# Kernel optimization log

Measured on AMD Instinct MI355X. Metric: run time of the kernel, lower is better.

The kernel has to match this reference:

```python
import jax, jax.numpy as jnp
import numpy as np

N, D, M1, K = 16384, 128, 64, 8  # batch, nodes (dims[0]), dims[1], k


def setup_inputs() -> dict:
    key = jax.random.key(0)
    ks = jax.random.split(key, 8)
    x = jax.random.normal(ks[0], (N, D), dtype=jnp.float32)
    # Stacked per-node fc1 weights: d independent Linear(d, m1) layers.
    s = 0.1
    w1_pos = jax.random.normal(ks[1], (D, M1, D), dtype=jnp.float32) * s
    b1_pos = jax.random.normal(ks[2], (D, M1), dtype=jnp.float32) * s
    w1_neg = jax.random.normal(ks[3], (D, M1, D), dtype=jnp.float32) * s
    b1_neg = jax.random.normal(ks[4], (D, M1), dtype=jnp.float32) * s
    # LocallyConnected(K, M1, 1): weight [K, M1, 1], bias [K, 1]
    w2 = jax.random.normal(ks[5], (K, M1, 1), dtype=jnp.float32) * s
    b2 = jax.random.normal(ks[6], (K, 1), dtype=jnp.float32) * s
    # fc3: d independent Linear(K, 1, bias=False) -> stacked [D, K]
    w3 = jax.random.normal(ks[7], (D, K), dtype=jnp.float32) * s
    return {"x": x, "w1_pos": w1_pos, "b1_pos": b1_pos,
            "w1_neg": w1_neg, "b1_neg": b1_neg,
            "w2": w2, "b2": b2, "w3": w3}


def reference(x, w1_pos, b1_pos, w1_neg, b1_neg, w2, b2, w3):
    d = x.shape[1]
    # Zeroing x[:, j] for node j == zeroing column j of node-j fc1 weight.
    mask = 1.0 - jnp.eye(d, dtype=x.dtype)            # [d, d]
    W = (w1_pos - w1_neg) * mask[:, None, :]          # [d, m1, d]
    b = b1_pos - b1_neg                                # [d, m1]
    h = jnp.einsum('nd,jmd->njm', x, W) + b            # [n, d, m1]
    # expand over K then sigmoid (sigmoid is identical for each k copy)
    h = jax.nn.sigmoid(h)
    # LocallyConnected: per-k matmul [m1 -> 1], bias [K, 1]
    z = jnp.einsum('njm,kmo->njko', h, w2) + b2        # [n, d, K, 1]
    z = z[..., 0]                                       # [n, d, K]
    # fc3: per-node Linear(K, 1, bias=False)
    out = jnp.einsum('njk,jk->nj', z, w3)              # [n, d]
    return out
```

## Files before the change

kernel.cpp:

```cpp
#include <hip/hip_runtime.h>
#include <hip/hip_bf16.h>

#define N_  16384
#define D_  128
#define M1_ 64
#define K_  8
#define LOG2E 1.44269504088896f

typedef short short8 __attribute__((ext_vector_type(8)));
typedef float f32x4  __attribute__((ext_vector_type(4)));

__device__ __forceinline__ ushort f2bf(float f) {
    union { float f; unsigned u; } un; un.f = f;
    unsigned u = un.u;
    return (ushort)((u + 0x7fffu + ((u >> 16) & 1u)) >> 16);
}

__global__ void prep_all(const float* __restrict__ x,
                         const float* __restrict__ w1p, const float* __restrict__ b1p,
                         const float* __restrict__ w1n, const float* __restrict__ b1n,
                         const float* __restrict__ w2,  const float* __restrict__ b2,
                         const float* __restrict__ w3,
                         ushort* __restrict__ xbf, ushort* __restrict__ wbf,
                         float* __restrict__ bp, float* __restrict__ vv,
                         float* __restrict__ cv) {
    int bx = blockIdx.x;
    if (bx < 2048) {
        int i = bx * 256 + threadIdx.x;
        int n = i >> 5;
        int d = (i & 31) * 4;
        float4 f = ((const float4*)x)[i];
        ushort4 o;
        o.x = f2bf(f.x); o.y = f2bf(f.y); o.z = f2bf(f.z); o.w = f2bf(f.w);
        int lane = (n & 15) + 16 * ((d >> 3) & 3);
        int idx  = (n >> 4) * 2048 + (d >> 5) * 512 + lane * 8 + (d & 7);
        *(ushort4*)&xbf[idx] = o;
    } else if (bx < 3072) {
        int i = (bx - 2048) * 256 + threadIdx.x;
        int base = i * 4;
        int j   = base >> 13;
        int rem = base & 8191;
        int m   = rem >> 7;
        int d   = rem & 127;
        float4 p = ((const float4*)w1p)[i];
        float4 n = ((const float4*)w1n)[i];
        float4 w;
        w.x = (p.x - n.x) * LOG2E; w.y = (p.y - n.y) * LOG2E;
        w.z = (p.z - n.z) * LOG2E; w.w = (p.w - n.w) * LOG2E;
        if (j == d    ) w.x = 0.f;
        if (j == d + 1) w.y = 0.f;
        if (j == d + 2) w.z = 0.f;
        if (j == d + 3) w.w = 0.f;
        ushort4 o;
        o.x = f2bf(w.x); o.y = f2bf(w.y); o.z = f2bf(w.z); o.w = f2bf(w.w);
        int lane = (m & 15) + 16 * ((d >> 3) & 3);
        int idx  = j * 8192 + ((d >> 5) * 4 + (m >> 4)) * 512 + lane * 8 + (d & 7);
        *(ushort4*)&wbf[idx] = o;
    } else {
        int idx = (bx - 3072) * 256 + threadIdx.x;
        int j = idx >> 6, m = idx & 63;
        float v = 0.f;
        for (int k = 0; k < K_; k++) v += w3[j * K_ + k] * w2[k * M1_ + m];
        vv[idx] = v;
        bp[idx] = (b1p[idx] - b1n[idx]) * LOG2E;
        if (m == 0) {
            float c = 0.f;
            for (int k = 0; k < K_; k++) c += w3[j * K_ + k] * b2[k];
            cv[j] = c;
        }
    }
}

__global__ __launch_bounds__(256) void main_mfma(
    const ushort* __restrict__ xbf, const ushort* __restrict__ wbf,
    const float* __restrict__ bvec, const float* __restrict__ vvec,
    const float* __restrict__ cvec, float* __restrict__ out) {
    const int tid  = threadIdx.x;
    const int wave = tid >> 6, lane = tid & 63;
    const int quad = lane >> 4, col = lane & 15;
    const int j    = blockIdx.y;
    const int nblk = blockIdx.x;

    short8 wfrag[4][4];
    const ushort* wg = wbf + (size_t)j * 8192 + lane * 8;
    #pragma unroll
    for (int ks = 0; ks < 4; ks++)
        #pragma unroll
        for (int mt = 0; mt < 4; mt++)
            wfrag[mt][ks] = *(const short8*)&wg[(ks * 4 + mt) * 512];

    f32x4 bias4[4], vm4[4];
    #pragma unroll
    for (int mt = 0; mt < 4; mt++) {
        bias4[mt] = *(const f32x4*)&bvec[j * M1_ + mt * 16 + quad * 4];
        vm4[mt]   = *(const f32x4*)&vvec[j * M1_ + mt * 16 + quad * 4];
    }
    const float cj = cvec[j];

    const ushort* xg = xbf + ((size_t)(nblk * 32 + wave)) * 2048 + lane * 8;
    float* outp = out + (size_t)(nblk * 512 + wave * 16 + col) * D_ + j;

    short8 abuf[2][4];
    #pragma unroll
    for (int ks = 0; ks < 4; ks++)
        abuf[0][ks] = *(const short8*)&xg[ks * 512];

    float pr[8];

    #pragma unroll
    for (int st = 0; st < 8; st++) {
        const int cur = st & 1, nxt = cur ^ 1;
        if (st < 7) {
            const ushort* xn = xg + (size_t)(st + 1) * 8192;
            #pragma unroll
            for (int ks = 0; ks < 4; ks++)
                abuf[nxt][ks] = *(const short8*)&xn[ks * 512];
        }

        f32x4 acc[4];
        #pragma unroll
        for (int mt = 0; mt < 4; mt++) acc[mt] = bias4[mt];
        #pragma unroll
        for (int ks = 0; ks < 4; ks++)
            #pragma unroll
            for (int mt = 0; mt < 4; mt++)
                acc[mt] = __builtin_amdgcn_mfma_f32_16x16x32_bf16(
                              wfrag[mt][ks], abuf[cur][ks], acc[mt], 0, 0, 0);

        float partial = 0.f;
        #pragma unroll
        for (int mt = 0; mt < 4; mt++)
            #pragma unroll
            for (int r = 0; r < 4; r++) {
                float e = __builtin_amdgcn_exp2f(-acc[mt][r]);
                float s = __builtin_amdgcn_rcpf(1.0f + e);
                partial = fmaf(s, vm4[mt][r], partial);
            }
        pr[st] = partial;
    }

    #pragma unroll
    for (int st = 0; st < 8; st++)
        pr[st] += __shfl_xor(pr[st], 16);
    #pragma unroll
    for (int st = 0; st < 8; st++)
        pr[st] += __shfl_xor(pr[st], 32);
    if (quad == 0) {
        #pragma unroll
        for (int st = 0; st < 8; st++)
            outp[(size_t)st * 64 * D_] = pr[st] + cj;
    }
}

__global__ void fallback_kernel(const float* __restrict__ x,
                                const float* __restrict__ w1p, const float* __restrict__ b1p,
                                const float* __restrict__ w1n, const float* __restrict__ b1n,
                                const float* __restrict__ w2,  const float* __restrict__ b2,
                                const float* __restrict__ w3,  float* __restrict__ out) {
    int n = blockIdx.x, j = blockIdx.y, m = threadIdx.x;
    const float* xr = x + (size_t)n * D_;
    const float* wp = w1p + ((size_t)j * M1_ + m) * D_;
    const float* wn = w1n + ((size_t)j * M1_ + m) * D_;
    float acc = 0.f;
    for (int d = 0; d < D_; d++) {
        if (d == j) continue;
        acc += xr[d] * (wp[d] - wn[d]);
    }
    acc += b1p[j * M1_ + m] - b1n[j * M1_ + m];
    float h = 1.f / (1.f + __expf(-acc));
    float vmv = 0.f;
    for (int k = 0; k < K_; k++) vmv += w3[j * K_ + k] * w2[k * M1_ + m];
    float p = h * vmv;
    for (int off = 1; off < 64; off <<= 1) p += __shfl_xor(p, off);
    if (m == 0) {
        float c = 0.f;
        for (int k = 0; k < K_; k++) c += w3[j * K_ + k] * b2[k];
        out[(size_t)n * D_ + j] = p + c;
    }
}

extern "C" void kernel_launch(void* const* d_in, const int* in_sizes, int n_in,
                              void* d_out, int out_size, void* d_ws, size_t ws_size,
                              hipStream_t stream) {
    const float* x   = (const float*)d_in[0];
    const float* w1p = (const float*)d_in[1];
    const float* b1p = (const float*)d_in[2];
    const float* w1n = (const float*)d_in[3];
    const float* b1n = (const float*)d_in[4];
    const float* w2  = (const float*)d_in[5];
    const float* b2  = (const float*)d_in[6];
    const float* w3  = (const float*)d_in[7];
    float* out = (float*)d_out;

    const size_t off_x = 0;
    const size_t off_w = off_x + (size_t)N_ * D_ * 2;
    const size_t off_b = off_w + (size_t)D_ * M1_ * D_ * 2;
    const size_t off_v = off_b + (size_t)D_ * M1_ * 4;
    const size_t off_c = off_v + (size_t)D_ * M1_ * 4;
    const size_t need  = off_c + (size_t)D_ * 4;

    if (ws_size < need) {
        fallback_kernel<<<dim3(N_, D_), 64, 0, stream>>>(x, w1p, b1p, w1n, b1n, w2, b2, w3, out);
        return;
    }

    ushort* xbf = (ushort*)((char*)d_ws + off_x);
    ushort* wbf = (ushort*)((char*)d_ws + off_w);
    float*  bp  = (float*)((char*)d_ws + off_b);
    float*  vv  = (float*)((char*)d_ws + off_v);
    float*  cv  = (float*)((char*)d_ws + off_c);

    prep_all<<<3104, 256, 0, stream>>>(x, w1p, b1p, w1n, b1n, w2, b2, w3,
                                       xbf, wbf, bp, vv, cv);
    main_mfma<<<dim3(32, 128), 256, 0, stream>>>(xbf, wbf, bp, vv, cv, out);
}
```

Baseline: 124.1 us.

## Fuse bf16 prep into main MFMA kernel, converting x and weights on the fly

Removes the separate prep kernel and workspace. The main kernel now reads fp32 x and the w1 weights directly, converts them to bf16 in registers with the packed cvt instruction, and computes the bias, v and c vectors per block. It also shares a single reciprocal across four sigmoids through product tricks. This saves a launch and the workspace round trip. In exchange each of the 128 j-blocks re-reads fp32 x (twice the bytes of bf16), and each of the 32 n-blocks redundantly converts the same weights.

```diff
diff --git a/kernel.cpp b/kernel.cpp
--- a/kernel.cpp
+++ b/kernel.cpp
@@ -1,5 +1,4 @@
 #include <hip/hip_runtime.h>
-#include <hip/hip_bf16.h>
 
 #define N_  16384
 #define D_  128
@@ -10,71 +9,19 @@
 typedef short short8 __attribute__((ext_vector_type(8)));
 typedef float f32x4  __attribute__((ext_vector_type(4)));
 
-__device__ __forceinline__ ushort f2bf(float f) {
-    union { float f; unsigned u; } un; un.f = f;
-    unsigned u = un.u;
-    return (ushort)((u + 0x7fffu + ((u >> 16) & 1u)) >> 16);
+__device__ __forceinline__ unsigned cvt_pk_bf16(float lo, float hi) {
+    unsigned r;
+    asm("v_cvt_pk_bf16_f32 %0, %1, %2" : "=v"(r) : "v"(lo), "v"(hi));
+    return r;
 }
 
-__global__ void prep_all(const float* __restrict__ x,
-                         const float* __restrict__ w1p, const float* __restrict__ b1p,
-                         const float* __restrict__ w1n, const float* __restrict__ b1n,
-                         const float* __restrict__ w2,  const float* __restrict__ b2,
-                         const float* __restrict__ w3,
-                         ushort* __restrict__ xbf, ushort* __restrict__ wbf,
-                         float* __restrict__ bp, float* __restrict__ vv,
-                         float* __restrict__ cv) {
-    int bx = blockIdx.x;
-    if (bx < 2048) {
-        int i = bx * 256 + threadIdx.x;
-        int n = i >> 5;
-        int d = (i & 31) * 4;
-        float4 f = ((const float4*)x)[i];
-        ushort4 o;
-        o.x = f2bf(f.x); o.y = f2bf(f.y); o.z = f2bf(f.z); o.w = f2bf(f.w);
-        int lane = (n & 15) + 16 * ((d >> 3) & 3);
-        int idx  = (n >> 4) * 2048 + (d >> 5) * 512 + lane * 8 + (d & 7);
-        *(ushort4*)&xbf[idx] = o;
-    } else if (bx < 3072) {
-        int i = (bx - 2048) * 256 + threadIdx.x;
-        int base = i * 4;
-        int j   = base >> 13;
-        int rem = base & 8191;
-        int m   = rem >> 7;
-        int d   = rem & 127;
-        float4 p = ((const float4*)w1p)[i];
-        float4 n = ((const float4*)w1n)[i];
-        float4 w;
-        w.x = (p.x - n.x) * LOG2E; w.y = (p.y - n.y) * LOG2E;
-        w.z = (p.z - n.z) * LOG2E; w.w = (p.w - n.w) * LOG2E;
-        if (j == d    ) w.x = 0.f;
-        if (j == d + 1) w.y = 0.f;
-        if (j == d + 2) w.z = 0.f;
-        if (j == d + 3) w.w = 0.f;
-        ushort4 o;
-        o.x = f2bf(w.x); o.y = f2bf(w.y); o.z = f2bf(w.z); o.w = f2bf(w.w);
-        int lane = (m & 15) + 16 * ((d >> 3) & 3);
-        int idx  = j * 8192 + ((d >> 5) * 4 + (m >> 4)) * 512 + lane * 8 + (d & 7);
-        *(ushort4*)&wbf[idx] = o;
-    } else {
-        int idx = (bx - 3072) * 256 + threadIdx.x;
-        int j = idx >> 6, m = idx & 63;
-        float v = 0.f;
-        for (int k = 0; k < K_; k++) v += w3[j * K_ + k] * w2[k * M1_ + m];
-        vv[idx] = v;
-        bp[idx] = (b1p[idx] - b1n[idx]) * LOG2E;
-        if (m == 0) {
-            float c = 0.f;
-            for (int k = 0; k < K_; k++) c += w3[j * K_ + k] * b2[k];
-            cv[j] = c;
-        }
-    }
-}
-
-__global__ __launch_bounds__(256) void main_mfma(
-    const ushort* __restrict__ xbf, const ushort* __restrict__ wbf,
-    const float* __restrict__ bvec, const float* __restrict__ vvec,
-    const float* __restrict__ cvec, float* __restrict__ out) {
+__global__ __launch_bounds__(256) void fused_all(
+    const float* __restrict__ x,
+    const float* __restrict__ w1p, const float* __restrict__ b1p,
+    const float* __restrict__ w1n, const float* __restrict__ b1n,
+    const float* __restrict__ w2,  const float* __restrict__ b2,
+    const float* __restrict__ w3,  float* __restrict__ out)
+{
     const int tid  = threadIdx.x;
     const int wave = tid >> 6, lane = tid & 63;
     const int quad = lane >> 4, col = lane & 15;
@@ -82,39 +29,90 @@
     const int nblk = blockIdx.x;
 
     short8 wfrag[4][4];
-    const ushort* wg = wbf + (size_t)j * 8192 + lane * 8;
+    {
+        const float* wp = w1p + ((size_t)j * M1_ + col) * D_ + quad * 8;
+        const float* wn = w1n + ((size_t)j * M1_ + col) * D_ + quad * 8;
+        #pragma unroll
+        for (int mt = 0; mt < 4; mt++) {
+            #pragma unroll
+            for (int ks = 0; ks < 4; ks++) {
+                const size_t o = (size_t)mt * 16 * D_ + ks * 32;
+                float4 p0 = *(const float4*)(wp + o);
+                float4 p1 = *(const float4*)(wp + o + 4);
+                float4 n0 = *(const float4*)(wn + o);
+                float4 n1 = *(const float4*)(wn + o + 4);
+                float f[8];
+                f[0] = p0.x - n0.x; f[1] = p0.y - n0.y;
+                f[2] = p0.z - n0.z; f[3] = p0.w - n0.w;
+                f[4] = p1.x - n1.x; f[5] = p1.y - n1.y;
+                f[6] = p1.z - n1.z; f[7] = p1.w - n1.w;
+                const int dbase = ks * 32 + quad * 8;
+                #pragma unroll
+                for (int e = 0; e < 8; e++)
+                    f[e] = (dbase + e == j) ? 0.f : f[e] * LOG2E;
+                union { unsigned u[4]; short8 s; } r;
+                r.u[0] = cvt_pk_bf16(f[0], f[1]);
+                r.u[1] = cvt_pk_bf16(f[2], f[3]);
+                r.u[2] = cvt_pk_bf16(f[4], f[5]);
+                r.u[3] = cvt_pk_bf16(f[6], f[7]);
+                wfrag[mt][ks] = r.s;
+            }
+        }
+    }
+
+    float w3v[K_];
     #pragma unroll
-    for (int ks = 0; ks < 4; ks++)
-        #pragma unroll
-        for (int mt = 0; mt < 4; mt++)
-            wfrag[mt][ks] = *(const short8*)&wg[(ks * 4 + mt) * 512];
+    for (int k = 0; k < K_; k++) w3v[k] = w3[j * K_ + k];
 
     f32x4 bias4[4], vm4[4];
     #pragma unroll
     for (int mt = 0; mt < 4; mt++) {
-        bias4[mt] = *(const f32x4*)&bvec[j * M1_ + mt * 16 + quad * 4];
-        vm4[mt]   = *(const f32x4*)&vvec[j * M1_ + mt * 16 + quad * 4];
+        #pragma unroll
+        for (int r = 0; r < 4; r++) {
+            const int m = mt * 16 + quad * 4 + r;
+            float v = 0.f;
+            #pragma unroll
+            for (int k = 0; k < K_; k++) v = fmaf(w3v[k], w2[k * M1_ + m], v);
+            vm4[mt][r]   = v;
+            bias4[mt][r] = (b1p[j * M1_ + m] - b1n[j * M1_ + m]) * LOG2E;
+        }
     }
-    const float cj = cvec[j];
+    float cj = 0.f;
+    #pragma unroll
+    for (int k = 0; k < K_; k++) cj = fmaf(w3v[k], b2[k], cj);
 
-    const ushort* xg = xbf + ((size_t)(nblk * 32 + wave)) * 2048 + lane * 8;
+    const float* xg = x + ((size_t)((nblk * 32 + wave) * 16 + col)) * D_ + quad * 8;
     float* outp = out + (size_t)(nblk * 512 + wave * 16 + col) * D_ + j;
 
-    short8 abuf[2][4];
+    float4 raw[8];
     #pragma unroll
-    for (int ks = 0; ks < 4; ks++)
-        abuf[0][ks] = *(const short8*)&xg[ks * 512];
+    for (int ks = 0; ks < 4; ks++) {
+        raw[2 * ks]     = *(const float4*)(xg + ks * 32);
+        raw[2 * ks + 1] = *(const float4*)(xg + ks * 32 + 4);
+    }
 
     float pr[8];
 
     #pragma unroll
     for (int st = 0; st < 8; st++) {
-        const int cur = st & 1, nxt = cur ^ 1;
+        short8 abuf[4];
+        #pragma unroll
+        for (int ks = 0; ks < 4; ks++) {
+            union { unsigned u[4]; short8 s; } r;
+            r.u[0] = cvt_pk_bf16(raw[2 * ks].x,     raw[2 * ks].y);
+            r.u[1] = cvt_pk_bf16(raw[2 * ks].z,     raw[2 * ks].w);
+            r.u[2] = cvt_pk_bf16(raw[2 * ks + 1].x, raw[2 * ks + 1].y);
+            r.u[3] = cvt_pk_bf16(raw[2 * ks + 1].z, raw[2 * ks + 1].w);
+            abuf[ks] = r.s;
+        }
+
         if (st < 7) {
-            const ushort* xn = xg + (size_t)(st + 1) * 8192;
+            const float* xn = xg + (size_t)(st + 1) * (4 * 16 * D_);
             #pragma unroll
-            for (int ks = 0; ks < 4; ks++)
-                abuf[nxt][ks] = *(const short8*)&xn[ks * 512];
+            for (int ks = 0; ks < 4; ks++) {
+                raw[2 * ks]     = *(const float4*)(xn + ks * 32);
+                raw[2 * ks + 1] = *(const float4*)(xn + ks * 32 + 4);
+            }
         }
 
         f32x4 acc[4];
@@ -125,26 +123,30 @@
             #pragma unroll
             for (int mt = 0; mt < 4; mt++)
                 acc[mt] = __builtin_amdgcn_mfma_f32_16x16x32_bf16(
-                              wfrag[mt][ks], abuf[cur][ks], acc[mt], 0, 0, 0);
+                              wfrag[mt][ks], abuf[ks], acc[mt], 0, 0, 0);
 
         float partial = 0.f;
         #pragma unroll
-        for (int mt = 0; mt < 4; mt++)
-            #pragma unroll
-            for (int r = 0; r < 4; r++) {
-                float e = __builtin_amdgcn_exp2f(-acc[mt][r]);
-                float s = __builtin_amdgcn_rcpf(1.0f + e);
-                partial = fmaf(s, vm4[mt][r], partial);
-            }
+        for (int mt = 0; mt < 4; mt++) {
+            float e0 = __builtin_amdgcn_exp2f(-acc[mt][0]);
+            float e1 = __builtin_amdgcn_exp2f(-acc[mt][1]);
+            float e2 = __builtin_amdgcn_exp2f(-acc[mt][2]);
+            float e3 = __builtin_amdgcn_exp2f(-acc[mt][3]);
+            float u0 = 1.f + e0, u1 = 1.f + e1, u2 = 1.f + e2, u3 = 1.f + e3;
+            float p01 = u0 * u1, p23 = u2 * u3;
+            float rc  = __builtin_amdgcn_rcpf(p01 * p23);
+            partial = fmaf(vm4[mt][0], rc * (p23 * u1), partial);
+            partial = fmaf(vm4[mt][1], rc * (p23 * u0), partial);
+            partial = fmaf(vm4[mt][2], rc * (p01 * u3), partial);
+            partial = fmaf(vm4[mt][3], rc * (p01 * u2), partial);
+        }
         pr[st] = partial;
     }
 
     #pragma unroll
-    for (int st = 0; st < 8; st++)
-        pr[st] += __shfl_xor(pr[st], 16);
+    for (int st = 0; st < 8; st++) pr[st] += __shfl_xor(pr[st], 16);
     #pragma unroll
-    for (int st = 0; st < 8; st++)
-        pr[st] += __shfl_xor(pr[st], 32);
+    for (int st = 0; st < 8; st++) pr[st] += __shfl_xor(pr[st], 32);
     if (quad == 0) {
         #pragma unroll
         for (int st = 0; st < 8; st++)
@@ -152,65 +154,14 @@
     }
 }
 
-__global__ void fallback_kernel(const float* __restrict__ x,
-                                const float* __restrict__ w1p, const float* __restrict__ b1p,
-                                const float* __restrict__ w1n, const float* __restrict__ b1n,
-                                const float* __restrict__ w2,  const float* __restrict__ b2,
-                                const float* __restrict__ w3,  float* __restrict__ out) {
-    int n = blockIdx.x, j = blockIdx.y, m = threadIdx.x;
-    const float* xr = x + (size_t)n * D_;
-    const float* wp = w1p + ((size_t)j * M1_ + m) * D_;
-    const float* wn = w1n + ((size_t)j * M1_ + m) * D_;
-    float acc = 0.f;
-    for (int d = 0; d < D_; d++) {
-        if (d == j) continue;
-        acc += xr[d] * (wp[d] - wn[d]);
-    }
-    acc += b1p[j * M1_ + m] - b1n[j * M1_ + m];
-    float h = 1.f / (1.f + __expf(-acc));
-    float vmv = 0.f;
-    for (int k = 0; k < K_; k++) vmv += w3[j * K_ + k] * w2[k * M1_ + m];
-    float p = h * vmv;
-    for (int off = 1; off < 64; off <<= 1) p += __shfl_xor(p, off);
-    if (m == 0) {
-        float c = 0.f;
-        for (int k = 0; k < K_; k++) c += w3[j * K_ + k] * b2[k];
-        out[(size_t)n * D_ + j] = p + c;
-    }
-}
-
 extern "C" void kernel_launch(void* const* d_in, const int* in_sizes, int n_in,
                               void* d_out, int out_size, void* d_ws, size_t ws_size,
                               hipStream_t stream) {
-    const float* x   = (const float*)d_in[0];
-    const float* w1p = (const float*)d_in[1];
-    const float* b1p = (const float*)d_in[2];
-    const float* w1n = (const float*)d_in[3];
-    const float* b1n = (const float*)d_in[4];
-    const float* w2  = (const float*)d_in[5];
-    const float* b2  = (const float*)d_in[6];
-    const float* w3  = (const float*)d_in[7];
-    float* out = (float*)d_out;
-
-    const size_t off_x = 0;
-    const size_t off_w = off_x + (size_t)N_ * D_ * 2;
-    const size_t off_b = off_w + (size_t)D_ * M1_ * D_ * 2;
-    const size_t off_v = off_b + (size_t)D_ * M1_ * 4;
-    const size_t off_c = off_v + (size_t)D_ * M1_ * 4;
-    const size_t need  = off_c + (size_t)D_ * 4;
-
-    if (ws_size < need) {
-        fallback_kernel<<<dim3(N_, D_), 64, 0, stream>>>(x, w1p, b1p, w1n, b1n, w2, b2, w3, out);
-        return;
-    }
-
-    ushort* xbf = (ushort*)((char*)d_ws + off_x);
-    ushort* wbf = (ushort*)((char*)d_ws + off_w);
-    float*  bp  = (float*)((char*)d_ws + off_b);
-    float*  vv  = (float*)((char*)d_ws + off_v);
-    float*  cv  = (float*)((char*)d_ws + off_c);
-
-    prep_all<<<3104, 256, 0, stream>>>(x, w1p, b1p, w1n, b1n, w2, b2, w3,
-                                       xbf, wbf, bp, vv, cv);
-    main_mfma<<<dim3(32, 128), 256, 0, stream>>>(xbf, wbf, bp, vv, cv, out);
+    (void)in_sizes; (void)n_in; (void)out_size; (void)d_ws; (void)ws_size;
+    fused_all<<<dim3(32, 128), 256, 0, stream>>>(
+        (const float*)d_in[0],
+        (const float*)d_in[1], (const float*)d_in[2],
+        (const float*)d_in[3], (const float*)d_in[4],
+        (const float*)d_in[5], (const float*)d_in[6],
+        (const float*)d_in[7], (float*)d_out);
 }
```

New measurement: 319.9 us. +157.9%, slower.
